# Kernel tuning notes

Hardware: AMD Instinct MI355X
Metric: run time of the kernel (lower is better)

Reference implementation:

```python
import jax, jax.numpy as jnp
import numpy as np
from itertools import product

S0 = 384          # voxel grid size per max_data_size
N0 = 500_000      # active surface voxels
NF_IN, NF = 2, 16
EPS = 1e-4        # scn.BatchNormReLU default eps


def _make_nbr(lin, S, offs):
    # submanifold rulebook: nbr[k, i] = row of active neighbor of site i at offset k, else sentinel N
    N = len(lin)
    x = lin // (S * S); y = (lin // S) % S; z = lin % S
    nbr = np.full((len(offs), N), N, np.int32)
    for k, (dx, dy, dz) in enumerate(offs):
        nx, ny, nz = x + dx, y + dy, z + dz
        valid = (nx >= 0) & (nx < S) & (ny >= 0) & (ny < S) & (nz >= 0) & (nz < S)
        q = (nx * S + ny) * S + nz
        pos = np.minimum(np.searchsorted(lin, q), N - 1)
        nbr[k] = np.where(valid & (lin[pos] == q), pos, N).astype(np.int32)
    return nbr


def _downsample(lin, S):
    # half-resolution active sites, unpool parent map, and 2x2x2 stride-2 conv rulebook
    x = lin // (S * S); y = (lin // S) % S; z = lin % S
    Sh = S // 2
    plin = ((x // 2) * Sh + (y // 2)) * Sh + (z // 2)
    lin_h = np.unique(plin)
    parent = np.searchsorted(lin_h, plin).astype(np.int32)
    xh = lin_h // (Sh * Sh); yh = (lin_h // Sh) % Sh; zh = lin_h % Sh
    N, Nh = len(lin), len(lin_h)
    down = np.full((8, Nh), N, np.int32)
    for k, (ox, oy, oz) in enumerate(product((0, 1), repeat=3)):
        q = ((2 * xh + ox) * S + (2 * yh + oy)) * S + (2 * zh + oz)
        pos = np.minimum(np.searchsorted(lin, q), N - 1)
        down[k] = np.where(lin[pos] == q, pos, N).astype(np.int32)
    return lin_h, parent, down


def setup_inputs() -> dict:
    rng = np.random.default_rng(0)
    cand = rng.integers(0, S0 ** 3, size=int(N0 * 1.1))
    lin0 = np.unique(cand)[:N0]
    assert len(lin0) == N0
    offs27 = list(product((-1, 0, 1), repeat=3))
    nbr0 = _make_nbr(lin0, S0, offs27)
    lin1, parent01, down01 = _downsample(lin0, S0)
    nbr1 = _make_nbr(lin1, S0 // 2, offs27)
    lin2, parent12, down12 = _downsample(lin1, S0 // 2)
    nbr2 = _make_nbr(lin2, S0 // 4, offs27)

    key = jax.random.key(0)
    ks = jax.random.split(key, 16)
    n = lambda k, sh, sc: jax.random.normal(k, sh, jnp.float32) * sc
    return dict(
        feats=n(ks[0], (N0, NF_IN), 1.0),
        w_p1=n(ks[1], (27, NF_IN, NF), 1.0 / np.sqrt(27 * NF_IN)),
        blk_bn1_g=1.0 + n(ks[2], (3, NF), 0.1), blk_bn1_b=n(ks[3], (3, NF), 0.1),
        blk_w1=n(ks[4], (3, 27, NF, NF), 1.0 / np.sqrt(27 * NF)),
        blk_bn2_g=1.0 + n(ks[5], (3, NF), 0.1), blk_bn2_b=n(ks[6], (3, NF), 0.1),
        blk_w2=n(ks[7], (3, 27, NF, NF), 1.0 / np.sqrt(27 * NF)),
        down_bn_g=1.0 + n(ks[8], (2, NF), 0.1), down_bn_b=n(ks[9], (2, NF), 0.1),
        down_w=n(ks[10], (2, 8, NF, NF), 1.0 / np.sqrt(8 * NF)),
        bn3_g=1.0 + n(ks[11], (3 * NF,), 0.1), bn3_b=n(ks[12], (3 * NF,), 0.1),
        w_sdf=n(ks[13], (3 * NF, 1), 1.0 / np.sqrt(3 * NF)),
        b_sdf=jnp.zeros((1,), jnp.float32),
        nbr0=jnp.asarray(nbr0), nbr1=jnp.asarray(nbr1), nbr2=jnp.asarray(nbr2),
        down01=jnp.asarray(down01), down12=jnp.asarray(down12),
        parent01=jnp.asarray(parent01), parent12=jnp.asarray(parent12),
    )


def _sconv(x, nbr, W):
    # rulebook gather-GEMM-accumulate sparse conv.
    # x: [Nin, Cin], nbr: [K, Nout] (index Nin == inactive sentinel), W: [K, Cin, Cout]
    xp = jnp.concatenate([x, jnp.zeros((1, x.shape[1]), x.dtype)], 0)
    acc0 = jnp.zeros((nbr.shape[1], W.shape[2]), x.dtype)
    def step(acc, kw):
        idx, Wk = kw
        return acc + xp[idx] @ Wk, None
    out, _ = jax.lax.scan(step, acc0, (nbr, W))
    return out


def _bnrelu(x, g, b):
    # SCN BatchNorm: batch stats over active sites only
    m = x.mean(0); v = x.var(0)
    return jax.nn.relu((x - m) * jax.lax.rsqrt(v + EPS) * g + b)


def _res_block(x, nbr, g1, b1, w1, g2, b2, w2):
    # pre-activation residual block, identity skip (in == out channels)
    h = _sconv(_bnrelu(x, g1, b1), nbr, w1)
    h = _sconv(_bnrelu(h, g2, b2), nbr, w2)
    return x + h


def reference(feats, w_p1, blk_bn1_g, blk_bn1_b, blk_w1, blk_bn2_g, blk_bn2_b,
              blk_w2, down_bn_g, down_bn_b, down_w, bn3_g, bn3_b, w_sdf, b_sdf,
              nbr0, nbr1, nbr2, down01, down12, parent01, parent12):
    blk = lambda x, nbr, i: _res_block(x, nbr, blk_bn1_g[i], blk_bn1_b[i], blk_w1[i],
                                       blk_bn2_g[i], blk_bn2_b[i], blk_w2[i])
    x = _sconv(feats, nbr0, w_p1)                                    # p1: submanifold conv nf_in->nf
    r0 = blk(x, nbr0, 0)                                             # FCN level 0 block
    y1 = _sconv(_bnrelu(r0, down_bn_g[0], down_bn_b[0]), down01, down_w[0])  # stride-2 conv
    r1 = blk(y1, nbr1, 1)                                            # level 1 block
    z2 = _sconv(_bnrelu(r1, down_bn_g[1], down_bn_b[1]), down12, down_w[1])
    r2 = blk(z2, nbr2, 2)                                            # level 2 block
    j1 = jnp.concatenate([r1, r2[parent12]], axis=-1)                # UnPool + JoinTable -> 2*nf
    j0 = jnp.concatenate([r0, j1[parent01]], axis=-1)                # UnPool + JoinTable -> 3*nf
    h = _bnrelu(j0, bn3_g, bn3_b)                                    # p3
    return h @ w_sdf + b_sdf                                         # sdf linear, [N0, 1]
```

## Files before the change

kernel.cpp:

```cpp
#include <hip/hip_runtime.h>

#define BN_EPS 1e-4f
#define NREP 16

typedef _Float16 f16x8 __attribute__((ext_vector_type(8)));
typedef float f32x4 __attribute__((ext_vector_type(4)));

__global__ __launch_bounds__(256) void build_k(
    const int* __restrict__ nbr, int N, int Nin, int ngroups,
    int* __restrict__ gcnt, int* __restrict__ ent)
{
    const int wave = threadIdx.x >> 6, lane = threadIdx.x & 63;
    const int l15 = lane & 15, q = lane >> 4;

    for (int grp = blockIdx.x * 4 + wave; grp < ngroups; grp += gridDim.x * 4) {
        const int site = grp * 16 + l15;
        int v[7];
        unsigned act = 0;
#pragma unroll
        for (int p = 0; p < 7; ++p) {
            const int t = 4 * p + q;
            int idx = Nin;
            if (t < 27 && site < N) idx = nbr[(size_t)t * N + site];
            v[p] = idx;
            const unsigned long long bal = __ballot(idx < Nin);
#pragma unroll
            for (int qq = 0; qq < 4; ++qq) {
                const int tt = 4 * p + qq;
                if (tt < 27 && ((bal >> (16 * qq)) & 0xFFFFull)) act |= 1u << tt;
            }
        }
        const int cnt = __popc(act);
        if (lane == 0) gcnt[grp] = cnt;
        const int e0 = grp * 27;
#pragma unroll
        for (int p = 0; p < 7; ++p) {
            const int t = 4 * p + q;
            if (t < 27 && ((act >> t) & 1)) {
                const int e = __popc(act & ((1u << t) - 1));
                ent[(size_t)(e0 + e) * 16 + l15] = (v[p] << 5) | t;
            }
        }
    }
}

__global__ __launch_bounds__(256, 4) void conv16c_k(
    const float* __restrict__ act,
    const int* __restrict__ gcnt,
    const int* __restrict__ ent,
    const _Float16* __restrict__ WT,
    const float* __restrict__ g,
    const float* __restrict__ b,
    const float* __restrict__ stats_in,
    float invN,
    float* __restrict__ out,
    float* __restrict__ stats_out,
    int Nout, int Nin, int addSkip)
{
    __shared__ _Float16 WTs[27 * 2 * 16 * 8];
    __shared__ float TRS[4][16 * 20];
    __shared__ float RED[4][32];
    __shared__ float sbl[2][16];

    const int wave = threadIdx.x >> 6, lane = threadIdx.x & 63;
    const int l15 = lane & 15, q = lane >> 4;
    const int h = q & 1, th = q >> 1;
    const int SENT = Nin << 5;
    float* Tr = TRS[wave];

    {
        const float4* s = (const float4*)WT;
        float4* d = (float4*)WTs;
        for (int v = threadIdx.x; v < 27 * 2 * 16; v += 256) d[v] = s[v];
        if (threadIdx.x < 16) {
            const int c = threadIdx.x;
            float su = 0.f, sq = 0.f;
#pragma unroll
            for (int rep = 0; rep < NREP; ++rep) {
                su += stats_in[rep * 128 + c];
                sq += stats_in[rep * 128 + 64 + c];
            }
            const float mean = su * invN;
            const float var = sq * invN - mean * mean;
            const float sc = g[c] * rsqrtf(var + BN_EPS);
            sbl[0][c] = sc;
            sbl[1][c] = fmaf(-mean, sc, b[c]);
        }
    }
    __syncthreads();

    float scv[8], biv[8];
#pragma unroll
    for (int j = 0; j < 8; ++j) {
        scv[j] = sbl[0][h * 8 + j];
        biv[j] = sbl[1][h * 8 + j];
    }

    const int ngroups = (Nout + 15) >> 4;
    const int stride = gridDim.x * 4;
    const int rr = lane >> 2, cc = (lane & 3) * 4;
    float sj[4] = {0.f, 0.f, 0.f, 0.f}, qj[4] = {0.f, 0.f, 0.f, 0.f};

    int grp = blockIdx.x * 4 + wave;
    int cc_cur = 0, cc_nxt = 0;
    int pe[14];
    if (grp < ngroups) {
        cc_cur = gcnt[grp];
        const int g1 = grp + stride;
        if (g1 < ngroups) cc_nxt = gcnt[g1];
        const size_t e0 = (size_t)grp * 27;
#pragma unroll
        for (int pp = 0; pp < 14; ++pp) {
            const int sidx = 2 * pp + th;
            int r = SENT;
            if (sidx < cc_cur) r = ent[(e0 + sidx) * 16 + l15];
            pe[pp] = r;
        }
    }

    while (grp < ngroups) {
        int ce[14];
#pragma unroll
        for (int pp = 0; pp < 14; ++pp) ce[pp] = pe[pp];

        const int base = grp * 16, srow = base + rr;
        float4 skip = make_float4(0.f, 0.f, 0.f, 0.f);
        if (addSkip && srow < Nout)
            skip = *(const float4*)(out + (size_t)srow * 16 + cc);

        const int gn = grp + stride;
        int cc_nn = 0;
        if (gn < ngroups) {
            const size_t e0n = (size_t)gn * 27;
#pragma unroll
            for (int pp = 0; pp < 14; ++pp) {
                const int sidx = 2 * pp + th;
                int r = SENT;
                if (sidx < cc_nxt) r = ent[(e0n + sidx) * 16 + l15];
                pe[pp] = r;
            }
            const int gnn = gn + stride;
            if (gnn < ngroups) cc_nn = gcnt[gnn];
        }

        f32x4 acc0 = {0.f, 0.f, 0.f, 0.f}, acc1 = {0.f, 0.f, 0.f, 0.f};
#pragma unroll
        for (int pp = 0; pp < 14; ++pp) {
            const int raw = ce[pp];
            const int tap = raw & 31;
            f16x8 a = {};
            if (raw < SENT) {
                const float* rp = act + ((size_t)(raw >> 5) * 16 + h * 8);
                const float4 x0 = ((const float4*)rp)[0];
                const float4 x1 = ((const float4*)rp)[1];
                const float y[8] = {x0.x, x0.y, x0.z, x0.w,
                                    x1.x, x1.y, x1.z, x1.w};
#pragma unroll
                for (int j = 0; j < 8; ++j)
                    a[j] = (_Float16)fmaxf(fmaf(y[j], scv[j], biv[j]), 0.f);
            }
            const f16x8 bb = *(const f16x8*)(WTs + ((tap * 2 + h) * 16 + l15) * 8);
            if (pp & 1) acc1 = __builtin_amdgcn_mfma_f32_16x16x32_f16(a, bb, acc1, 0, 0, 0);
            else        acc0 = __builtin_amdgcn_mfma_f32_16x16x32_f16(a, bb, acc0, 0, 0, 0);
        }

#pragma unroll
        for (int r = 0; r < 4; ++r)
            Tr[(q * 4 + r) * 20 + l15] = acc0[r] + acc1[r];
        float4 v4;
        v4.x = Tr[rr * 20 + cc + 0] + skip.x;
        v4.y = Tr[rr * 20 + cc + 1] + skip.y;
        v4.z = Tr[rr * 20 + cc + 2] + skip.z;
        v4.w = Tr[rr * 20 + cc + 3] + skip.w;
        if (srow < Nout) {
            *(float4*)(out + (size_t)srow * 16 + cc) = v4;
            sj[0] += v4.x; qj[0] += v4.x * v4.x;
            sj[1] += v4.y; qj[1] += v4.y * v4.y;
            sj[2] += v4.z; qj[2] += v4.z * v4.z;
            sj[3] += v4.w; qj[3] += v4.w * v4.w;
        }
        cc_cur = cc_nxt; cc_nxt = cc_nn;
        grp = gn;
    }

    if (stats_out) {
#pragma unroll
        for (int m = 4; m < 64; m <<= 1) {
#pragma unroll
            for (int j = 0; j < 4; ++j) {
                sj[j] += __shfl_xor(sj[j], m);
                qj[j] += __shfl_xor(qj[j], m);
            }
        }
        if (lane < 4) {
#pragma unroll
            for (int j = 0; j < 4; ++j) {
                RED[wave][lane * 4 + j] = sj[j];
                RED[wave][16 + lane * 4 + j] = qj[j];
            }
        }
        __syncthreads();
        if (threadIdx.x < 32) {
            const int t2 = threadIdx.x;
            float* bank = stats_out + (blockIdx.x & (NREP - 1)) * 128;
            atomicAdd(bank + (t2 < 16 ? t2 : 48 + t2),
                      RED[0][t2] + RED[1][t2] + RED[2][t2] + RED[3][t2]);
        }
    }
}

template <int K>
__global__ __launch_bounds__(256, 4) void conv16_k(
    const float* __restrict__ act, const int* __restrict__ nbr,
    const _Float16* __restrict__ WB,
    const float* __restrict__ g, const float* __restrict__ b,
    const float* __restrict__ stats_in, float invN,
    float* __restrict__ out, float* __restrict__ stats_out,
    int Nout, int Nin, int addSkip)
{
    constexpr int PAIRS = (K + 1) / 2;
    __shared__ float sbl[2][16];
    const int wave = threadIdx.x >> 6, lane = threadIdx.x & 63;
    const int l15 = lane & 15, q = lane >> 4;
    const int h = q & 1, th = q >> 1;

    if (threadIdx.x < 16) {
        const int c = threadIdx.x;
        float su = 0.f, sq = 0.f;
#pragma unroll
        for (int rep = 0; rep < NREP; ++rep) {
            su += stats_in[rep * 128 + c];
            sq += stats_in[rep * 128 + 64 + c];
        }
        const float mean = su * invN;
        const float var = sq * invN - mean * mean;
        const float sc = g[c] * rsqrtf(var + BN_EPS);
        sbl[0][c] = sc;
        sbl[1][c] = fmaf(-mean, sc, b[c]);
    }
    __syncthreads();

    float scv[8], biv[8];
#pragma unroll
    for (int j = 0; j < 8; ++j) {
        scv[j] = sbl[0][h * 8 + j];
        biv[j] = sbl[1][h * 8 + j];
    }

    f16x8 bfr[PAIRS];
#pragma unroll
    for (int p = 0; p < PAIRS; ++p)
        bfr[p] = *(const f16x8*)(WB + ((size_t)p * 64 + lane) * 8);

    const int ngroups = (Nout + 15) >> 4;
    float s = 0.f, ss = 0.f;

    for (int grp = blockIdx.x * 4 + wave; grp < ngroups; grp += gridDim.x * 4) {
        const int base = grp * 16;
        const int site = min(base + l15, Nout - 1);
        int idxs[PAIRS];
#pragma unroll
        for (int p = 0; p < PAIRS; ++p) {
            const int t = 2 * p + ((2 * p + 1 < K) ? th : 0);
            idxs[p] = nbr[(size_t)t * Nout + site];
        }
        f32x4 acc0 = {0.f, 0.f, 0.f, 0.f}, acc1 = {0.f, 0.f, 0.f, 0.f};
#pragma unroll
        for (int p = 0; p < PAIRS; ++p) {
            const int idx = idxs[p];
            f16x8 a = {};
            if (idx < Nin) {
                const float* rp = act + ((size_t)idx * 16 + h * 8);
                const float4 x0 = ((const float4*)rp)[0];
                const float4 x1 = ((const float4*)rp)[1];
                const float y[8] = {x0.x, x0.y, x0.z, x0.w,
                                    x1.x, x1.y, x1.z, x1.w};
#pragma unroll
                for (int j = 0; j < 8; ++j)
                    a[j] = (_Float16)fmaxf(fmaf(y[j], scv[j], biv[j]), 0.f);
            }
            if (p & 1) acc1 = __builtin_amdgcn_mfma_f32_16x16x32_f16(a, bfr[p], acc1, 0, 0, 0);
            else       acc0 = __builtin_amdgcn_mfma_f32_16x16x32_f16(a, bfr[p], acc0, 0, 0, 0);
        }
#pragma unroll
        for (int r = 0; r < 4; ++r) {
            const int row = base + q * 4 + r;
            float v = acc0[r] + acc1[r];
            if (row < Nout) {
                float* op = out + (size_t)row * 16 + l15;
                if (addSkip) v += *op;
                *op = v;
                s += v; ss += v * v;
            }
        }
    }

    if (stats_out) {
        s  += __shfl_xor(s, 16);  s  += __shfl_xor(s, 32);
        ss += __shfl_xor(ss, 16); ss += __shfl_xor(ss, 32);
        __shared__ float red[4][32];
        if (lane < 16) { red[wave][l15] = s; red[wave][16 + l15] = ss; }
        __syncthreads();
        if (threadIdx.x < 32) {
            const int t2 = threadIdx.x;
            float* bank = stats_out + (blockIdx.x & (NREP - 1)) * 128;
            atomicAdd(bank + (t2 < 16 ? t2 : 48 + t2),
                      red[0][t2] + red[1][t2] + red[2][t2] + red[3][t2]);
        }
    }
}

__global__ __launch_bounds__(256, 4) void convp1_k(
    const float* __restrict__ feats,
    const int* __restrict__ nbr,
    const _Float16* __restrict__ WB,
    float* __restrict__ out, float* __restrict__ stats_out, int N)
{
    const int wave = threadIdx.x >> 6, lane = threadIdx.x & 63;
    const int l15 = lane & 15, q = lane >> 4;

    f16x8 b0 = *(const f16x8*)(WB + (size_t)lane * 8);
    f16x8 b1 = *(const f16x8*)(WB + ((size_t)64 + lane) * 8);

    const int ngroups = (N + 15) >> 4;
    float s = 0.f, ss = 0.f;

    for (int grp = blockIdx.x * 4 + wave; grp < ngroups; grp += gridDim.x * 4) {
        const int base = grp * 16;
        const int site = min(base + l15, N - 1);
        int tid[8];
#pragma unroll
        for (int u = 0; u < 8; ++u) {
            const int t = (u < 4) ? (q * 4 + u) : (16 + q * 4 + (u - 4));
            tid[u] = (t < 27) ? nbr[(size_t)t * N + site] : N;
        }
        f32x4 acc = {0.f, 0.f, 0.f, 0.f};
#pragma unroll
        for (int mf = 0; mf < 2; ++mf) {
            f16x8 a;
#pragma unroll
            for (int jt = 0; jt < 4; ++jt) {
                const int idx = tid[mf * 4 + jt];
                float2 f = make_float2(0.f, 0.f);
                if (idx < N) f = *(const float2*)(feats + (size_t)idx * 2);
                a[jt * 2] = (_Float16)f.x; a[jt * 2 + 1] = (_Float16)f.y;
            }
            acc = __builtin_amdgcn_mfma_f32_16x16x32_f16(a, mf ? b1 : b0, acc, 0, 0, 0);
        }
#pragma unroll
        for (int r = 0; r < 4; ++r) {
            const int row = base + q * 4 + r;
            const float v = acc[r];
            if (row < N) {
                out[(size_t)row * 16 + l15] = v;
                s += v; ss += v * v;
            }
        }
    }

    s  += __shfl_xor(s, 16);  s  += __shfl_xor(s, 32);
    ss += __shfl_xor(ss, 16); ss += __shfl_xor(ss, 32);
    __shared__ float red[4][32];
    if (lane < 16) { red[wave][l15] = s; red[wave][16 + l15] = ss; }
    __syncthreads();
    if (threadIdx.x < 32) {
        const int t2 = threadIdx.x;
        float* bank = stats_out + (blockIdx.x & (NREP - 1)) * 128;
        atomicAdd(bank + (t2 < 16 ? t2 : 48 + t2),
                  red[0][t2] + red[1][t2] + red[2][t2] + red[3][t2]);
    }
}

__global__ void pack_k(const float* __restrict__ w_p1, const float* __restrict__ w1,
                       const float* __restrict__ w2, const float* __restrict__ dw,
                       _Float16* __restrict__ WBp1, _Float16* __restrict__ WT27,
                       _Float16* __restrict__ WB8)
{
    const int b = blockIdx.x;
    if (b == 0) {
        for (int v = threadIdx.x; v < 2 * 64 * 8; v += 256) {
            const int mf = v >> 9, lane = (v >> 3) & 63, j = v & 7;
            const int qq = lane >> 4, n = lane & 15;
            const int kg = mf * 32 + qq * 8 + j;
            const int t = kg >> 1, cin = kg & 1;
            WBp1[v] = (t < 27) ? (_Float16)w_p1[t * 32 + cin * 16 + n] : (_Float16)0.f;
        }
    } else if (b <= 6) {
        const int ti = b - 1, lvl = ti >> 1;
        const float* src = ((ti & 1) ? w2 : w1) + lvl * 6912;
        _Float16* dst = WT27 + (size_t)ti * 6912;
        for (int v = threadIdx.x; v < 6912; v += 256) {
            const int j = v & 7, n = (v >> 3) & 15, hh = (v >> 7) & 1, t = v >> 8;
            dst[v] = (_Float16)src[t * 256 + (hh * 8 + j) * 16 + n];
        }
    } else {
        const int ti = b - 7;
        const float* src = dw + ti * 2048;
        _Float16* dst = WB8 + (size_t)ti * (4 * 64 * 8);
        for (int v = threadIdx.x; v < 4 * 64 * 8; v += 256) {
            const int p = v >> 9, lane = (v >> 3) & 63, j = v & 7;
            const int qq = lane >> 4, n = lane & 15;
            const int t = 2 * p + (qq >> 1);
            const int cin = (qq & 1) * 8 + j;
            dst[v] = (_Float16)src[t * 256 + cin * 16 + n];
        }
    }
}

__global__ void fin_k(float* __restrict__ stats, const float* __restrict__ g,
                      const float* __restrict__ b, float* __restrict__ sb,
                      int C, float invN)
{
    const int c = threadIdx.x;
    if (c < C) {
        float su = 0.f, sq = 0.f;
#pragma unroll
        for (int rep = 0; rep < NREP; ++rep) {
            su += stats[rep * 128 + c];
            sq += stats[rep * 128 + 64 + c];
        }
        const float mean = su * invN;
        const float var = sq * invN - mean * mean;
        const float s = g[c] * rsqrtf(var + BN_EPS);
        sb[c] = s;
        sb[64 + c] = fmaf(-mean, s, b[c]);
    }
}

__device__ __forceinline__ float wred(float v) {
#pragma unroll
    for (int off = 32; off > 0; off >>= 1) v += __shfl_xor(v, off);
    return v;
}

__global__ __launch_bounds__(256) void gstats_k(
    const float* __restrict__ R0, const float* __restrict__ R1,
    const float* __restrict__ R2, const int* __restrict__ p01,
    const int* __restrict__ p12, float* __restrict__ stats, int N0)
{
    float s[48], q[48];
#pragma unroll
    for (int c = 0; c < 48; ++c) { s[c] = 0.f; q[c] = 0.f; }

    for (int n = blockIdx.x * blockDim.x + threadIdx.x; n < N0;
         n += gridDim.x * blockDim.x) {
        const int i1 = p01[n];
        const int i2 = p12[i1];
        const float4* a0 = (const float4*)(R0 + (size_t)n * 16);
        const float4* a1 = (const float4*)(R1 + (size_t)i1 * 16);
        const float4* a2 = (const float4*)(R2 + (size_t)i2 * 16);
#pragma unroll
        for (int j = 0; j < 4; ++j) {
            const float4 v = a0[j]; const int c = 4 * j;
            s[c] += v.x; q[c] += v.x * v.x; s[c+1] += v.y; q[c+1] += v.y * v.y;
            s[c+2] += v.z; q[c+2] += v.z * v.z; s[c+3] += v.w; q[c+3] += v.w * v.w;
        }
#pragma unroll
        for (int j = 0; j < 4; ++j) {
            const float4 v = a1[j]; const int c = 16 + 4 * j;
            s[c] += v.x; q[c] += v.x * v.x; s[c+1] += v.y; q[c+1] += v.y * v.y;
            s[c+2] += v.z; q[c+2] += v.z * v.z; s[c+3] += v.w; q[c+3] += v.w * v.w;
        }
#pragma unroll
        for (int j = 0; j < 4; ++j) {
            const float4 v = a2[j]; const int c = 32 + 4 * j;
            s[c] += v.x; q[c] += v.x * v.x; s[c+1] += v.y; q[c+1] += v.y * v.y;
            s[c+2] += v.z; q[c+2] += v.z * v.z; s[c+3] += v.w; q[c+3] += v.w * v.w;
        }
    }

    __shared__ float red[4][96];
    const int wave = threadIdx.x >> 6, lane = threadIdx.x & 63;
#pragma unroll
    for (int c = 0; c < 48; ++c) {
        const float ss = wred(s[c]);
        const float qq = wred(q[c]);
        if (lane == 0) { red[wave][c] = ss; red[wave][48 + c] = qq; }
    }
    __syncthreads();
    const int t = threadIdx.x;
    if (t < 96) {
        float* bank = stats + (blockIdx.x & (NREP - 1)) * 128;
        const float v = red[0][t] + red[1][t] + red[2][t] + red[3][t];
        atomicAdd(bank + (t < 48 ? t : 64 + (t - 48)), v);
    }
}

__global__ __launch_bounds__(256) void out_k(
    const float* __restrict__ R0, const float* __restrict__ R1,
    const float* __restrict__ R2, const int* __restrict__ p01,
    const int* __restrict__ p12, const float* __restrict__ sb,
    const float* __restrict__ wsdf, const float* __restrict__ bsdf,
    float* __restrict__ out, int N0)
{
    const int n = blockIdx.x * 256 + threadIdx.x;
    if (n >= N0) return;
    const int i1 = p01[n];
    const int i2 = p12[i1];
    float acc = bsdf[0];
    const float4* a0 = (const float4*)(R0 + (size_t)n * 16);
    const float4* a1 = (const float4*)(R1 + (size_t)i1 * 16);
    const float4* a2 = (const float4*)(R2 + (size_t)i2 * 16);
#pragma unroll
    for (int j = 0; j < 4; ++j) {
        const float4 v = a0[j]; const int c = 4 * j;
        acc += fmaxf(fmaf(v.x, sb[c+0], sb[64+c+0]), 0.f) * wsdf[c+0];
        acc += fmaxf(fmaf(v.y, sb[c+1], sb[64+c+1]), 0.f) * wsdf[c+1];
        acc += fmaxf(fmaf(v.z, sb[c+2], sb[64+c+2]), 0.f) * wsdf[c+2];
        acc += fmaxf(fmaf(v.w, sb[c+3], sb[64+c+3]), 0.f) * wsdf[c+3];
    }
#pragma unroll
    for (int j = 0; j < 4; ++j) {
        const float4 v = a1[j]; const int c = 16 + 4 * j;
        acc += fmaxf(fmaf(v.x, sb[c+0], sb[64+c+0]), 0.f) * wsdf[c+0];
        acc += fmaxf(fmaf(v.y, sb[c+1], sb[64+c+1]), 0.f) * wsdf[c+1];
        acc += fmaxf(fmaf(v.z, sb[c+2], sb[64+c+2]), 0.f) * wsdf[c+2];
        acc += fmaxf(fmaf(v.w, sb[c+3], sb[64+c+3]), 0.f) * wsdf[c+3];
    }
#pragma unroll
    for (int j = 0; j < 4; ++j) {
        const float4 v = a2[j]; const int c = 32 + 4 * j;
        acc += fmaxf(fmaf(v.x, sb[c+0], sb[64+c+0]), 0.f) * wsdf[c+0];
        acc += fmaxf(fmaf(v.y, sb[c+1], sb[64+c+1]), 0.f) * wsdf[c+1];
        acc += fmaxf(fmaf(v.z, sb[c+2], sb[64+c+2]), 0.f) * wsdf[c+2];
        acc += fmaxf(fmaf(v.w, sb[c+3], sb[64+c+3]), 0.f) * wsdf[c+3];
    }
    out[n] = acc;
}

extern "C" void kernel_launch(void* const* d_in, const int* in_sizes, int n_in,
                              void* d_out, int out_size, void* d_ws, size_t ws_size,
                              hipStream_t stream)
{
    const float* feats = (const float*)d_in[0];
    const float* w_p1  = (const float*)d_in[1];
    const float* bn1g  = (const float*)d_in[2];
    const float* bn1b  = (const float*)d_in[3];
    const float* w1    = (const float*)d_in[4];
    const float* bn2g  = (const float*)d_in[5];
    const float* bn2b  = (const float*)d_in[6];
    const float* w2    = (const float*)d_in[7];
    const float* dbng  = (const float*)d_in[8];
    const float* dbnb  = (const float*)d_in[9];
    const float* dw    = (const float*)d_in[10];
    const float* bn3g  = (const float*)d_in[11];
    const float* bn3b  = (const float*)d_in[12];
    const float* wsdf  = (const float*)d_in[13];
    const float* bsdf  = (const float*)d_in[14];
    const int* nbr0    = (const int*)d_in[15];
    const int* nbr1    = (const int*)d_in[16];
    const int* nbr2    = (const int*)d_in[17];
    const int* down01  = (const int*)d_in[18];
    const int* down12  = (const int*)d_in[19];
    const int* p01     = (const int*)d_in[20];
    const int* p12     = (const int*)d_in[21];

    const int N0 = in_sizes[0] / 2;
    const int N1 = in_sizes[18] / 8;
    const int N2 = in_sizes[19] / 8;
    const int ng0 = (N0 + 15) / 16, ng1 = (N1 + 15) / 16, ng2 = (N2 + 15) / 16;
    const int maxe = ng0 * 27 + 64;

    char* wp = (char*)d_ws;
    auto alloc = [&](size_t bytes) { char* r = wp; wp += (bytes + 255) & ~(size_t)255; return r; };
    float* T  = (float*)alloc((size_t)N0 * 16 * 4);
    float* R0 = (float*)alloc((size_t)N0 * 16 * 4);
    float* R1 = (float*)alloc((size_t)N1 * 16 * 4);
    float* R2 = (float*)alloc((size_t)N2 * 16 * 4);
    float* st = (float*)alloc(9 * NREP * 128 * 4);
    float* sb = (float*)alloc(128 * 4);
    _Float16* WBp1 = (_Float16*)alloc(2 * 64 * 8 * 2);
    _Float16* WT27 = (_Float16*)alloc(6 * 6912 * 2);
    _Float16* WB8  = (_Float16*)alloc(2 * 4 * 64 * 8 * 2);
    int* gcnt = (int*)alloc((size_t)ng0 * 4);
    int* ent  = (int*)alloc((size_t)maxe * 16 * 4);

    hipMemsetAsync(st, 0, 9 * NREP * 128 * sizeof(float), stream);

    const dim3 B(256);
    auto cgrid = [](int n) {
        const int g = (((n + 15) / 16) + 3) / 4;
        return dim3((unsigned)(g < 2048 ? g : 2048));
    };
    auto lgrid = [](int n) { return dim3((unsigned)((n + 255) / 256)); };
    const float i0 = 1.0f / N0, i1 = 1.0f / N1, i2 = 1.0f / N2;
    auto S = [&](int i) { return st + i * NREP * 128; };
    auto WT = [&](int i) { return WT27 + (size_t)i * 6912; };
    auto W8 = [&](int i) { return WB8 + (size_t)i * (4 * 64 * 8); };

    pack_k<<<9, B, 0, stream>>>(w_p1, w1, w2, dw, WBp1, WT27, WB8);

    build_k<<<cgrid(N0), B, 0, stream>>>(nbr0, N0, N0, ng0, gcnt, ent);
    convp1_k<<<cgrid(N0), B, 0, stream>>>(feats, nbr0, WBp1, R0, S(0), N0);
    conv16c_k<<<cgrid(N0), B, 0, stream>>>(R0, gcnt, ent, WT(0), bn1g, bn1b,
                                           S(0), i0, T, S(1), N0, N0, 0);
    conv16c_k<<<cgrid(N0), B, 0, stream>>>(T, gcnt, ent, WT(1), bn2g, bn2b,
                                           S(1), i0, R0, S(2), N0, N0, 1);
    conv16_k<8><<<cgrid(N1), B, 0, stream>>>(R0, down01, W8(0), dbng, dbnb,
                                             S(2), i0, R1, S(3), N1, N0, 0);

    build_k<<<cgrid(N1), B, 0, stream>>>(nbr1, N1, N1, ng1, gcnt, ent);
    conv16c_k<<<cgrid(N1), B, 0, stream>>>(R1, gcnt, ent, WT(2), bn1g + 16, bn1b + 16,
                                           S(3), i1, T, S(4), N1, N1, 0);
    conv16c_k<<<cgrid(N1), B, 0, stream>>>(T, gcnt, ent, WT(3), bn2g + 16, bn2b + 16,
                                           S(4), i1, R1, S(5), N1, N1, 1);
    conv16_k<8><<<cgrid(N2), B, 0, stream>>>(R1, down12, W8(1), dbng + 16, dbnb + 16,
                                             S(5), i1, R2, S(6), N2, N1, 0);

    build_k<<<cgrid(N2), B, 0, stream>>>(nbr2, N2, N2, ng2, gcnt, ent);
    conv16c_k<<<cgrid(N2), B, 0, stream>>>(R2, gcnt, ent, WT(4), bn1g + 32, bn1b + 32,
                                           S(6), i2, T, S(7), N2, N2, 0);
    conv16c_k<<<cgrid(N2), B, 0, stream>>>(T, gcnt, ent, WT(5), bn2g + 32, bn2b + 32,
                                           S(7), i2, R2, nullptr, N2, N2, 1);

    gstats_k<<<512, B, 0, stream>>>(R0, R1, R2, p01, p12, S(8), N0);
    fin_k<<<1, 64, 0, stream>>>(S(8), bn3g, bn3b, sb, 48, i0);
    out_k<<<lgrid(N0), B, 0, stream>>>(R0, R1, R2, p01, p12, sb, wsdf, bsdf,
                                       (float*)d_out, N0);
}
```

Baseline: 642.0 us.

## Gather fp16 shadow activations in sparse convs and apply BN-ReLU in packed half

Each conv kernel now also writes an fp16 copy of its output, and the next conv gathers neighbor rows from that half-precision copy instead of the fp32 tensor. This halves the bytes per random gather, which dominate the rulebook convolutions. The BN scale/bias and ReLU are now done with packed fp16 vector math rather than per-element fp32 FMAs. The cost is extra fp16 stores from every conv, and some precision loss because BN is applied in half precision after a round-to-zero conversion.

```diff
diff --git a/kernel.cpp b/kernel.cpp
--- a/kernel.cpp
+++ b/kernel.cpp
@@ -4,6 +4,8 @@
 #define NREP 16
 
 typedef _Float16 f16x8 __attribute__((ext_vector_type(8)));
+typedef __fp16 h8 __attribute__((ext_vector_type(8)));
+typedef __fp16 h2 __attribute__((ext_vector_type(2)));
 typedef float f32x4 __attribute__((ext_vector_type(4)));
 
 __global__ __launch_bounds__(256) void build_k(
@@ -45,7 +47,7 @@
 }
 
 __global__ __launch_bounds__(256, 4) void conv16c_k(
-    const float* __restrict__ act,
+    const __fp16* __restrict__ H,
     const int* __restrict__ gcnt,
     const int* __restrict__ ent,
     const _Float16* __restrict__ WT,
@@ -54,6 +56,7 @@
     const float* __restrict__ stats_in,
     float invN,
     float* __restrict__ out,
+    __fp16* __restrict__ Hout,
     float* __restrict__ stats_out,
     int Nout, int Nin, int addSkip)
 {
@@ -89,11 +92,12 @@
     }
     __syncthreads();
 
-    float scv[8], biv[8];
+    h8 sc8, bi8;
+    const h8 z8 = {};
 #pragma unroll
     for (int j = 0; j < 8; ++j) {
-        scv[j] = sbl[0][h * 8 + j];
-        biv[j] = sbl[1][h * 8 + j];
+        sc8[j] = (__fp16)sbl[0][h * 8 + j];
+        bi8[j] = (__fp16)sbl[1][h * 8 + j];
     }
 
     const int ngroups = (Nout + 15) >> 4;
@@ -148,17 +152,12 @@
         for (int pp = 0; pp < 14; ++pp) {
             const int raw = ce[pp];
             const int tap = raw & 31;
-            f16x8 a = {};
+            h8 ah = {};
             if (raw < SENT) {
-                const float* rp = act + ((size_t)(raw >> 5) * 16 + h * 8);
-                const float4 x0 = ((const float4*)rp)[0];
-                const float4 x1 = ((const float4*)rp)[1];
-                const float y[8] = {x0.x, x0.y, x0.z, x0.w,
-                                    x1.x, x1.y, x1.z, x1.w};
-#pragma unroll
-                for (int j = 0; j < 8; ++j)
-                    a[j] = (_Float16)fmaxf(fmaf(y[j], scv[j], biv[j]), 0.f);
-            }
+                ah = *(const h8*)((const char*)H + (raw & ~31) + h * 16);
+                ah = __builtin_elementwise_max(ah * sc8 + bi8, z8);
+            }
+            const f16x8 a = __builtin_bit_cast(f16x8, ah);
             const f16x8 bb = *(const f16x8*)(WTs + ((tap * 2 + h) * 16 + l15) * 8);
             if (pp & 1) acc1 = __builtin_amdgcn_mfma_f32_16x16x32_f16(a, bb, acc1, 0, 0, 0);
             else        acc0 = __builtin_amdgcn_mfma_f32_16x16x32_f16(a, bb, acc0, 0, 0, 0);
@@ -174,6 +173,11 @@
         v4.w = Tr[rr * 20 + cc + 3] + skip.w;
         if (srow < Nout) {
             *(float4*)(out + (size_t)srow * 16 + cc) = v4;
+            if (Hout) {
+                h2* hp = (h2*)(Hout + (size_t)srow * 16 + cc);
+                hp[0] = __builtin_amdgcn_cvt_pkrtz(v4.x, v4.y);
+                hp[1] = __builtin_amdgcn_cvt_pkrtz(v4.z, v4.w);
+            }
             sj[0] += v4.x; qj[0] += v4.x * v4.x;
             sj[1] += v4.y; qj[1] += v4.y * v4.y;
             sj[2] += v4.z; qj[2] += v4.z * v4.z;
@@ -211,12 +215,12 @@
 
 template <int K>
 __global__ __launch_bounds__(256, 4) void conv16_k(
-    const float* __restrict__ act, const int* __restrict__ nbr,
+    const __fp16* __restrict__ H, const int* __restrict__ nbr,
     const _Float16* __restrict__ WB,
     const float* __restrict__ g, const float* __restrict__ b,
     const float* __restrict__ stats_in, float invN,
-    float* __restrict__ out, float* __restrict__ stats_out,
-    int Nout, int Nin, int addSkip)
+    float* __restrict__ out, __fp16* __restrict__ Hout,
+    float* __restrict__ stats_out, int Nout, int Nin, int addSkip)
 {
     constexpr int PAIRS = (K + 1) / 2;
     __shared__ float sbl[2][16];
@@ -240,11 +244,12 @@
     }
     __syncthreads();
 
-    float scv[8], biv[8];
+    h8 sc8, bi8;
+    const h8 z8 = {};
 #pragma unroll
     for (int j = 0; j < 8; ++j) {
-        scv[j] = sbl[0][h * 8 + j];
-        biv[j] = sbl[1][h * 8 + j];
+        sc8[j] = (__fp16)sbl[0][h * 8 + j];
+        bi8[j] = (__fp16)sbl[1][h * 8 + j];
     }
 
     f16x8 bfr[PAIRS];
@@ -268,17 +273,12 @@
 #pragma unroll
         for (int p = 0; p < PAIRS; ++p) {
             const int idx = idxs[p];
-            f16x8 a = {};
+            h8 ah = {};
             if (idx < Nin) {
-                const float* rp = act + ((size_t)idx * 16 + h * 8);
-                const float4 x0 = ((const float4*)rp)[0];
-                const float4 x1 = ((const float4*)rp)[1];
-                const float y[8] = {x0.x, x0.y, x0.z, x0.w,
-                                    x1.x, x1.y, x1.z, x1.w};
-#pragma unroll
-                for (int j = 0; j < 8; ++j)
-                    a[j] = (_Float16)fmaxf(fmaf(y[j], scv[j], biv[j]), 0.f);
-            }
+                ah = *(const h8*)(H + (size_t)idx * 16 + h * 8);
+                ah = __builtin_elementwise_max(ah * sc8 + bi8, z8);
+            }
+            const f16x8 a = __builtin_bit_cast(f16x8, ah);
             if (p & 1) acc1 = __builtin_amdgcn_mfma_f32_16x16x32_f16(a, bfr[p], acc1, 0, 0, 0);
             else       acc0 = __builtin_amdgcn_mfma_f32_16x16x32_f16(a, bfr[p], acc0, 0, 0, 0);
         }
@@ -290,6 +290,7 @@
                 float* op = out + (size_t)row * 16 + l15;
                 if (addSkip) v += *op;
                 *op = v;
+                if (Hout) Hout[(size_t)row * 16 + l15] = (__fp16)v;
                 s += v; ss += v * v;
             }
         }
@@ -314,7 +315,8 @@
     const float* __restrict__ feats,
     const int* __restrict__ nbr,
     const _Float16* __restrict__ WB,
-    float* __restrict__ out, float* __restrict__ stats_out, int N)
+    float* __restrict__ out, __fp16* __restrict__ Hout,
+    float* __restrict__ stats_out, int N)
 {
     const int wave = threadIdx.x >> 6, lane = threadIdx.x & 63;
     const int l15 = lane & 15, q = lane >> 4;
@@ -353,6 +355,7 @@
             const float v = acc[r];
             if (row < N) {
                 out[(size_t)row * 16 + l15] = v;
+                Hout[(size_t)row * 16 + l15] = (__fp16)v;
                 s += v; ss += v * v;
             }
         }
@@ -567,6 +570,8 @@
     float* R0 = (float*)alloc((size_t)N0 * 16 * 4);
     float* R1 = (float*)alloc((size_t)N1 * 16 * 4);
     float* R2 = (float*)alloc((size_t)N2 * 16 * 4);
+    __fp16* HA = (__fp16*)alloc((size_t)(N0 + 16) * 16 * 2);
+    __fp16* HB = (__fp16*)alloc((size_t)(N0 + 16) * 16 * 2);
     float* st = (float*)alloc(9 * NREP * 128 * 4);
     float* sb = (float*)alloc(128 * 4);
     _Float16* WBp1 = (_Float16*)alloc(2 * 64 * 8 * 2);
@@ -591,27 +596,27 @@
     pack_k<<<9, B, 0, stream>>>(w_p1, w1, w2, dw, WBp1, WT27, WB8);
 
     build_k<<<cgrid(N0), B, 0, stream>>>(nbr0, N0, N0, ng0, gcnt, ent);
-    convp1_k<<<cgrid(N0), B, 0, stream>>>(feats, nbr0, WBp1, R0, S(0), N0);
-    conv16c_k<<<cgrid(N0), B, 0, stream>>>(R0, gcnt, ent, WT(0), bn1g, bn1b,
-                                           S(0), i0, T, S(1), N0, N0, 0);
-    conv16c_k<<<cgrid(N0), B, 0, stream>>>(T, gcnt, ent, WT(1), bn2g, bn2b,
-                                           S(1), i0, R0, S(2), N0, N0, 1);
-    conv16_k<8><<<cgrid(N1), B, 0, stream>>>(R0, down01, W8(0), dbng, dbnb,
-                                             S(2), i0, R1, S(3), N1, N0, 0);
+    convp1_k<<<cgrid(N0), B, 0, stream>>>(feats, nbr0, WBp1, R0, HA, S(0), N0);
+    conv16c_k<<<cgrid(N0), B, 0, stream>>>(HA, gcnt, ent, WT(0), bn1g, bn1b,
+                                           S(0), i0, T, HB, S(1), N0, N0, 0);
+    conv16c_k<<<cgrid(N0), B, 0, stream>>>(HB, gcnt, ent, WT(1), bn2g, bn2b,
+                                           S(1), i0, R0, HA, S(2), N0, N0, 1);
+    conv16_k<8><<<cgrid(N1), B, 0, stream>>>(HA, down01, W8(0), dbng, dbnb,
+                                             S(2), i0, R1, HB, S(3), N1, N0, 0);
 
     build_k<<<cgrid(N1), B, 0, stream>>>(nbr1, N1, N1, ng1, gcnt, ent);
-    conv16c_k<<<cgrid(N1), B, 0, stream>>>(R1, gcnt, ent, WT(2), bn1g + 16, bn1b + 16,
-                                           S(3), i1, T, S(4), N1, N1, 0);
-    conv16c_k<<<cgrid(N1), B, 0, stream>>>(T, gcnt, ent, WT(3), bn2g + 16, bn2b + 16,
-                                           S(4), i1, R1, S(5), N1, N1, 1);
-    conv16_k<8><<<cgrid(N2), B, 0, stream>>>(R1, down12, W8(1), dbng + 16, dbnb + 16,
-                                             S(5), i1, R2, S(6), N2, N1, 0);
+    conv16c_k<<<cgrid(N1), B, 0, stream>>>(HB, gcnt, ent, WT(2), bn1g + 16, bn1b + 16,
+                                           S(3), i1, T, HA, S(4), N1, N1, 0);
+    conv16c_k<<<cgrid(N1), B, 0, stream>>>(HA, gcnt, ent, WT(3), bn2g + 16, bn2b + 16,
+                                           S(4), i1, R1, HB, S(5), N1, N1, 1);
+    conv16_k<8><<<cgrid(N2), B, 0, stream>>>(HB, down12, W8(1), dbng + 16, dbnb + 16,
+                                             S(5), i1, R2, HA, S(6), N2, N1, 0);
 
     build_k<<<cgrid(N2), B, 0, stream>>>(nbr2, N2, N2, ng2, gcnt, ent);
-    conv16c_k<<<cgrid(N2), B, 0, stream>>>(R2, gcnt, ent, WT(4), bn1g + 32, bn1b + 32,
-                                           S(6), i2, T, S(7), N2, N2, 0);
-    conv16c_k<<<cgrid(N2), B, 0, stream>>>(T, gcnt, ent, WT(5), bn2g + 32, bn2b + 32,
-                                           S(7), i2, R2, nullptr, N2, N2, 1);
+    conv16c_k<<<cgrid(N2), B, 0, stream>>>(HA, gcnt, ent, WT(4), bn1g + 32, bn1b + 32,
+                                           S(6), i2, T, HB, S(7), N2, N2, 0);
+    conv16c_k<<<cgrid(N2), B, 0, stream>>>(HB, gcnt, ent, WT(5), bn2g + 32, bn2b + 32,
+                                           S(7), i2, R2, nullptr, nullptr, N2, N2, 1);
 
     gstats_k<<<512, B, 0, stream>>>(R0, R1, R2, p01, p12, S(8), N0);
     fin_k<<<1, 64, 0, stream>>>(S(8), bn3g, bn3b, sb, 48, i0);
```

Result: no change. 634.0 us (-1.2%).
